# Performance work log

Measured on AMD Instinct MI355X. Metric: run time of the kernel, lower is better.

Reference implementation:

```python
import jax, jax.numpy as jnp
import numpy as np

NUM_HEADS = 16
HEAD_DIM = 64
MAX_MEM = 4 * 4096
TOP_K = 8
EPS = 1e-8


def _l2norm(x, eps=EPS):
    # matches torch F.normalize(p=2, dim=-1, eps): x / max(||x||, eps)
    n = jnp.sqrt(jnp.sum(x * x, axis=-1, keepdims=True))
    return x / jnp.maximum(n, eps)


def setup_inputs() -> dict:
    key0 = jax.random.key(0)
    ks = jax.random.split(key0, 8)
    B, S, D = 2, 512, 1024
    H, hd = NUM_HEADS, HEAD_DIM
    return {
        "inputs": jax.random.normal(ks[0], (B, S, D), dtype=jnp.float32),
        "query": jax.random.normal(ks[1], (B, H, S, hd), dtype=jnp.float32),
        "key": jax.random.normal(ks[2], (B, H, S, hd), dtype=jnp.float32),
        "value": jax.random.normal(ks[3], (B, H, S, hd), dtype=jnp.float32),
        "outputs": jax.random.normal(ks[4], (B, H, S, hd), dtype=jnp.float32),
        "gate": jnp.zeros((H,), dtype=jnp.float32),  # nn.Parameter init zeros
        "key_memories": jax.random.normal(ks[5], (H, MAX_MEM, hd), dtype=jnp.float32),
        "value_memories": jax.random.normal(ks[6], (H, MAX_MEM, hd), dtype=jnp.float32),
    }


def reference(inputs, query, key, value, outputs, gate, key_memories, value_memories):
    B, S, _ = inputs.shape
    H = query.shape[1]
    hd = HEAD_DIM

    # [B,H,S,d] -> [H, B*S, d]
    q = jnp.transpose(query, (1, 0, 2, 3)).reshape(H, B * S, hd)

    # --- KNN lookup (no_grad in original) ---
    qn = _l2norm(q)                    # [H, N, d]
    kn = _l2norm(key_memories)         # [H, M, d]
    sims = jnp.einsum("hnd,hmd->hnm", qn, kn) / jnp.sqrt(jnp.float32(hd))
    scores, indices = jax.lax.top_k(sims, TOP_K)  # [H, N, k]

    # gather memory values per head: [H, N, k, d]
    mem_vals = jax.vmap(lambda vm, ix: vm[ix])(value_memories, indices)

    # weighted sum over k neighbors
    weighted = jnp.sum(mem_vals * scores[..., None], axis=2)  # [H, N, d]
    weighted = weighted.reshape(H, B, S, hd).transpose(1, 0, 2, 3)  # [B,H,S,d]

    g = jax.nn.sigmoid(gate).reshape(1, H, 1, 1)
    out_dim = outputs.shape[-1]
    combined = g * weighted[..., :out_dim] + (1.0 - g) * outputs
    return combined
```

## Files before the change

### kernel.cpp

```cpp
#include <hip/hip_runtime.h>
#include <math.h>

#define NHEADS 16
#define HD 64
#define MMEM 16384
#define NQ 1024
#define SEQ 512
#define EPS 1e-8f
#define NPART 16
#define NT 32
#define NGRP 32
#define CMAX 8

typedef short bf16x8 __attribute__((ext_vector_type(8)));
typedef float f32x16 __attribute__((ext_vector_type(16)));

__device__ inline unsigned short f2bf(float f) {
    unsigned int u = __builtin_bit_cast(unsigned int, f);
    unsigned int r = (u + 0x7FFFu + ((u >> 16) & 1u)) >> 16;
    return (unsigned short)r;
}

#define SS(Q) (Q.x*Q.x + Q.y*Q.y + Q.z*Q.z + Q.w*Q.w)

__global__ __launch_bounds__(256)
void kprep_kernel(const float* __restrict__ kmem,
                  float* __restrict__ knr,
                  unsigned short* __restrict__ kbf) {
    __shared__ float ssl[256];
    const int tid = threadIdx.x;
    const int gid = blockIdx.x * 256 + tid;
    const int lane = gid & 63;
    const int ks   = (gid >> 6) & 3;
    const int t    = (gid >> 8) & 511;
    const int h    = gid >> 17;
    const int r    = lane & 31;
    const int hi   = lane >> 5;
    const int row  = t * 32 + r;
    const int d0   = ks * 16 + hi * 8;

    const float* src = kmem + (((size_t)h * MMEM + row) << 6) + d0;
    float4 v0 = *(const float4*)(src);
    float4 v1 = *(const float4*)(src + 4);
    ssl[tid] = SS(v0) + SS(v1);
    __syncthreads();
    float tot = ssl[r +   0] + ssl[r +  32] + ssl[r +  64] + ssl[r +  96]
              + ssl[r + 128] + ssl[r + 160] + ssl[r + 192] + ssl[r + 224];
    const float rn = 1.0f / fmaxf(sqrtf(tot), EPS);
    if (tid < 32) knr[h * MMEM + row] = rn;

    uint4 o;
    o.x = (unsigned)f2bf(v0.x * rn) | ((unsigned)f2bf(v0.y * rn) << 16);
    o.y = (unsigned)f2bf(v0.z * rn) | ((unsigned)f2bf(v0.w * rn) << 16);
    o.z = (unsigned)f2bf(v1.x * rn) | ((unsigned)f2bf(v1.y * rn) << 16);
    o.w = (unsigned)f2bf(v1.z * rn) | ((unsigned)f2bf(v1.w * rn) << 16);
    *(uint4*)(kbf + (size_t)gid * 8) = o;
}

__device__ inline float max16v(const f32x16& a) {
    float m0 = fmaxf(fmaxf(a[0],  a[1]),  a[2]);
    float m1 = fmaxf(fmaxf(a[3],  a[4]),  a[5]);
    float m2 = fmaxf(fmaxf(a[6],  a[7]),  a[8]);
    float m3 = fmaxf(fmaxf(a[9],  a[10]), a[11]);
    float m4 = fmaxf(fmaxf(a[12], a[13]), a[14]);
    float n0 = fmaxf(fmaxf(m0, m1), m2);
    float n1 = fmaxf(fmaxf(m3, m4), a[15]);
    return fmaxf(n0, n1);
}

__device__ inline void ins8(float (&tv)[8], float v) {
#pragma unroll
    for (int j = 0; j < 8; ++j) {
        float h_ = fmaxf(tv[j], v);
        float l_ = fminf(tv[j], v);
        tv[j] = h_;
        v = l_;
    }
}

__device__ inline void ins8u64(unsigned long long (&tv)[8], unsigned long long v) {
#pragma unroll
    for (int j = 0; j < 8; ++j) {
        unsigned long long h_ = tv[j] > v ? tv[j] : v;
        unsigned long long l_ = tv[j] > v ? v : tv[j];
        tv[j] = h_;
        v = l_;
    }
}

__device__ inline bf16x8 pack8f(float4 a, float4 b) {
    bf16x8 f;
    f[0] = (short)f2bf(a.x); f[1] = (short)f2bf(a.y);
    f[2] = (short)f2bf(a.z); f[3] = (short)f2bf(a.w);
    f[4] = (short)f2bf(b.x); f[5] = (short)f2bf(b.y);
    f[6] = (short)f2bf(b.z); f[7] = (short)f2bf(b.w);
    return f;
}

#define MFMA8Z(ACCA, ACCB, A0, A1, A2, A3)                                    \
    f32x16 ACCA = __builtin_amdgcn_mfma_f32_32x32x16_bf16(A0, qA[0], z16, 0,0,0); \
    f32x16 ACCB = __builtin_amdgcn_mfma_f32_32x32x16_bf16(A0, qB[0], z16, 0,0,0); \
    ACCA = __builtin_amdgcn_mfma_f32_32x32x16_bf16(A1, qA[1], ACCA, 0, 0, 0); \
    ACCB = __builtin_amdgcn_mfma_f32_32x32x16_bf16(A1, qB[1], ACCB, 0, 0, 0); \
    ACCA = __builtin_amdgcn_mfma_f32_32x32x16_bf16(A2, qA[2], ACCA, 0, 0, 0); \
    ACCB = __builtin_amdgcn_mfma_f32_32x32x16_bf16(A2, qB[2], ACCB, 0, 0, 0); \
    ACCA = __builtin_amdgcn_mfma_f32_32x32x16_bf16(A3, qA[3], ACCA, 0, 0, 0); \
    ACCB = __builtin_amdgcn_mfma_f32_32x32x16_bf16(A3, qB[3], ACCB, 0, 0, 0);

__global__ __launch_bounds__(64, 4)
void scanA_kernel(const float* __restrict__ query,
                  const unsigned short* __restrict__ kbf,
                  float* __restrict__ pmax) {
    const int lane = threadIdx.x;
    int bid = blockIdx.x;
    const int p  = bid & 15;  bid >>= 4;
    const int qg = bid & 15;  bid >>= 4;
    const int h  = bid;
    const int col = lane & 31;
    const int hi  = lane >> 5;
    const int n0  = qg * 64 + col;
    const int n1  = n0 + 32;

    bf16x8 qA[4], qB[4];
    {
        const int b0 = n0 >> 9, s0 = n0 & 511;
        const int b1 = n1 >> 9, s1 = n1 & 511;
        const float* qp0 = query + ((((size_t)b0 * NHEADS + h) * SEQ + s0) << 6);
        const float* qp1 = query + ((((size_t)b1 * NHEADS + h) * SEQ + s1) << 6);
#pragma unroll
        for (int ks = 0; ks < 4; ++ks) {
            const int d0 = ks * 16 + hi * 8;
            qA[ks] = pack8f(*(const float4*)(qp0 + d0), *(const float4*)(qp0 + d0 + 4));
            qB[ks] = pack8f(*(const float4*)(qp1 + d0), *(const float4*)(qp1 + d0 + 4));
        }
    }

    const f32x16 z16 = {0,0,0,0,0,0,0,0,0,0,0,0,0,0,0,0};
    float gA = -1e30f, gB = -1e30f;

    const unsigned char* ptr = (const unsigned char*)kbf
        + ((size_t)h * 512 + (size_t)p * NT) * 4096 + (size_t)lane * 16;

    bf16x8 aX0, aX1, aX2, aX3, aY0, aY1, aY2, aY3;
    aX0 = *(const bf16x8*)(ptr);
    aX1 = *(const bf16x8*)(ptr + 1024);
    aX2 = *(const bf16x8*)(ptr + 2048);
    aX3 = *(const bf16x8*)(ptr + 3072);

#pragma unroll 1
    for (int t = 0; t < NT; t += 2) {
        {
            const unsigned char* pn = ptr + (size_t)(t + 1) * 4096;
            aY0 = *(const bf16x8*)(pn);
            aY1 = *(const bf16x8*)(pn + 1024);
            aY2 = *(const bf16x8*)(pn + 2048);
            aY3 = *(const bf16x8*)(pn + 3072);
        }
        {
            MFMA8Z(accA, accB, aX0, aX1, aX2, aX3)
            gA = fmaxf(gA, max16v(accA));
            gB = fmaxf(gB, max16v(accB));
        }
        if (t + 2 < NT) {
            const unsigned char* p2 = ptr + (size_t)(t + 2) * 4096;
            aX0 = *(const bf16x8*)(p2);
            aX1 = *(const bf16x8*)(p2 + 1024);
            aX2 = *(const bf16x8*)(p2 + 2048);
            aX3 = *(const bf16x8*)(p2 + 3072);
        }
        {
            MFMA8Z(accC, accD, aY0, aY1, aY2, aY3)
            gA = fmaxf(gA, max16v(accC));
            gB = fmaxf(gB, max16v(accD));
        }
    }

    pmax[(((size_t)h * NQ + n0) << 5) + p * 2 + hi] = gA;
    pmax[(((size_t)h * NQ + n1) << 5) + p * 2 + hi] = gB;
}

__global__ __launch_bounds__(256)
void taured_kernel(const float* __restrict__ pmax,
                   float* __restrict__ tauv) {
    const int gid = blockIdx.x * 256 + threadIdx.x;
    float tv[8];
#pragma unroll
    for (int j = 0; j < 8; ++j) tv[j] = -1e30f;
#pragma unroll
    for (int k = 0; k < NGRP; ++k) ins8(tv, pmax[((size_t)gid << 5) + k]);
    tauv[gid] = tv[7];
}

__global__ __launch_bounds__(64, 4)
void scanB_kernel(const float* __restrict__ query,
                  const unsigned short* __restrict__ kbf,
                  const float* __restrict__ tauv,
                  unsigned* __restrict__ pcand,
                  unsigned* __restrict__ pcnt) {
    const int lane = threadIdx.x;
    int bid = blockIdx.x;
    const int p  = bid & 15;  bid >>= 4;
    const int qg = bid & 15;  bid >>= 4;
    const int h  = bid;
    const int col = lane & 31;
    const int hi  = lane >> 5;
    const int n0  = qg * 64 + col;
    const int n1  = n0 + 32;

    bf16x8 qA[4], qB[4];
    float ssA = 0.f, ssB = 0.f;
    {
        const int b0 = n0 >> 9, s0 = n0 & 511;
        const int b1 = n1 >> 9, s1 = n1 & 511;
        const float* qp0 = query + ((((size_t)b0 * NHEADS + h) * SEQ + s0) << 6);
        const float* qp1 = query + ((((size_t)b1 * NHEADS + h) * SEQ + s1) << 6);
#pragma unroll
        for (int ks = 0; ks < 4; ++ks) {
            const int d0 = ks * 16 + hi * 8;
            float4 a0 = *(const float4*)(qp0 + d0), b0v = *(const float4*)(qp0 + d0 + 4);
            float4 a1 = *(const float4*)(qp1 + d0), b1v = *(const float4*)(qp1 + d0 + 4);
            ssA += SS(a0) + SS(b0v);
            ssB += SS(a1) + SS(b1v);
            qA[ks] = pack8f(a0, b0v);
            qB[ks] = pack8f(a1, b1v);
        }
    }
    ssA += __shfl_xor(ssA, 32);
    ssB += __shfl_xor(ssB, 32);
    const float tA = tauv[h * NQ + n0] - (sqrtf(ssA) * 0.0078125f + 0.01f);
    const float tB = tauv[h * NQ + n1] - (sqrtf(ssB) * 0.0078125f + 0.01f);

    const f32x16 z16 = {0,0,0,0,0,0,0,0,0,0,0,0,0,0,0,0};

    const unsigned char* ptr = (const unsigned char*)kbf
        + ((size_t)h * 512 + (size_t)p * NT) * 4096 + (size_t)lane * 16;

    unsigned cA = 0, cB = 0;
    const size_t chA = (((size_t)h * NQ + n0) << 5) + p * 2 + hi;
    const size_t chB = (((size_t)h * NQ + n1) << 5) + p * 2 + hi;
    unsigned* mApt = pcand + chA * CMAX;
    unsigned* mBpt = pcand + chB * CMAX;

#define EMITG(ACC, TAU, C, LST, MBV) do {                                     \
        const float _g = max16v(ACC);                                         \
        if (_g >= (TAU)) {                                                    \
            unsigned _msk = 0;                                                \
            _Pragma("unroll")                                                 \
            for (int _r = 0; _r < 16; ++_r)                                   \
                _msk |= (ACC[_r] >= (TAU)) ? (1u << _r) : 0u;                 \
            do {                                                              \
                int _r = __ffs(_msk) - 1;                                     \
                unsigned _idx = (unsigned)((MBV) + (_r & 3) + 8 * (_r >> 2)); \
                if ((C) < CMAX) (LST)[C] = _idx;                              \
                ++(C);                                                        \
                _msk &= _msk - 1;                                             \
            } while (_msk);                                                   \
        }                                                                     \
    } while (0)

    bf16x8 aX0, aX1, aX2, aX3, aY0, aY1, aY2, aY3;
    aX0 = *(const bf16x8*)(ptr);
    aX1 = *(const bf16x8*)(ptr + 1024);
    aX2 = *(const bf16x8*)(ptr + 2048);
    aX3 = *(const bf16x8*)(ptr + 3072);

#pragma unroll 1
    for (int t = 0; t < NT; t += 2) {
        {
            const unsigned char* pn = ptr + (size_t)(t + 1) * 4096;
            aY0 = *(const bf16x8*)(pn);
            aY1 = *(const bf16x8*)(pn + 1024);
            aY2 = *(const bf16x8*)(pn + 2048);
            aY3 = *(const bf16x8*)(pn + 3072);
        }
        {
            MFMA8Z(accA, accB, aX0, aX1, aX2, aX3)
            const int mbv = p * 1024 + t * 32 + 4 * hi;
            EMITG(accA, tA, cA, mApt, mbv);
            EMITG(accB, tB, cB, mBpt, mbv);
        }
        if (t + 2 < NT) {
            const unsigned char* p2 = ptr + (size_t)(t + 2) * 4096;
            aX0 = *(const bf16x8*)(p2);
            aX1 = *(const bf16x8*)(p2 + 1024);
            aX2 = *(const bf16x8*)(p2 + 2048);
            aX3 = *(const bf16x8*)(p2 + 3072);
        }
        {
            MFMA8Z(accC, accD, aY0, aY1, aY2, aY3)
            const int mbv = p * 1024 + (t + 1) * 32 + 4 * hi;
            EMITG(accC, tA, cA, mApt, mbv);
            EMITG(accD, tB, cB, mBpt, mbv);
        }
    }
    pcnt[chA] = cA;
    pcnt[chB] = cB;
#undef EMITG
}

__global__ __launch_bounds__(64, 8)
void rescore_merge_kernel(const float* __restrict__ query,
                          const float* __restrict__ kmem,
                          const float* __restrict__ knr,
                          const unsigned* __restrict__ pcand,
                          const unsigned* __restrict__ pcnt,
                          const float* __restrict__ vmem,
                          const float* __restrict__ outputs,
                          const float* __restrict__ gate,
                          float* __restrict__ out) {
    __shared__ unsigned cands[NGRP * CMAX];
    const int gid = blockIdx.x;
    const int h = gid >> 10;
    const int n = gid & 1023;
    const int b = n >> 9;
    const int s = n & 511;
    const int lane = threadIdx.x;
    const int d4 = lane & 15;
    const int d5 = lane & 31;

    const float* qbase = query + ((((size_t)b * NHEADS + h) * SEQ + s) << 6);
    const float4 q4 = ((const float4*)qbase)[d4];
    float ssp = SS(q4);
    ssp += __shfl_xor(ssp, 1);
    ssp += __shfl_xor(ssp, 2);
    ssp += __shfl_xor(ssp, 4);
    ssp += __shfl_xor(ssp, 8);
    const float qs = 1.0f / (fmaxf(sqrtf(ssp), EPS) * 8.0f);

    const unsigned cg = pcnt[((size_t)gid << 5) + d5];
    const bool anyovf = (__ballot(cg > CMAX) != 0ULL);
    unsigned inc = cg;
#pragma unroll
    for (int d = 1; d < 32; d <<= 1) {
        unsigned t = __shfl_up(inc, d, 32);
        if (d5 >= d) inc += t;
    }
    const unsigned ct = __shfl(inc, 31, 32);
    const unsigned excl = inc - cg;
    if (lane < 32) {
        const unsigned* lp = pcand + (((size_t)gid << 5) + lane) * CMAX;
        const unsigned cc = cg > CMAX ? CMAX : cg;
        for (unsigned c = 0; c < cc; ++c) cands[excl + c] = lp[c];
    }
    __syncthreads();

    const float* kb = kmem + ((size_t)h << 20);
    const float* nb = knr + h * MMEM;

    unsigned long long top[8];
#pragma unroll
    for (int j = 0; j < 8; ++j) top[j] = 0ULL;

#define SCORE_KEY(IDX) ({                                                     \
        float4 kv = ((const float4*)(kb + ((size_t)(IDX) << 6)))[d4];         \
        float d = q4.x*kv.x + q4.y*kv.y + q4.z*kv.z + q4.w*kv.w;              \
        d += __shfl_xor(d, 1);                                                \
        d += __shfl_xor(d, 2);                                                \
        d += __shfl_xor(d, 4);                                                \
        d += __shfl_xor(d, 8);                                                \
        const float sc = d * qs * nb[IDX];                                    \
        unsigned su = __builtin_bit_cast(unsigned, sc);                       \
        unsigned ms = su ^ ((su >> 31) ? 0xFFFFFFFFu : 0x80000000u);          \
        ((unsigned long long)ms << 32) | (0xFFFFFFFFu - (unsigned)(IDX));     \
    })

    if (!anyovf) {
#pragma unroll 1
        for (unsigned c = 0; c < ct; ++c) {
            const unsigned idx = cands[c];
            ins8u64(top, SCORE_KEY(idx));
        }
    } else {
#pragma unroll 1
        for (int m = 0; m < MMEM; ++m) ins8u64(top, SCORE_KEY(m));
    }
#undef SCORE_KEY

    float acc = 0.0f;
    const float* vb = vmem + ((size_t)h << 20);
#pragma unroll
    for (int j = 0; j < 8; ++j) {
        const unsigned long long key = top[j];
        const unsigned idx = 0xFFFFFFFFu - (unsigned)(key & 0xFFFFFFFFu);
        const unsigned ms = (unsigned)(key >> 32);
        const unsigned su = ms ^ ((ms >> 31) ? 0x80000000u : 0xFFFFFFFFu);
        const float sc = __builtin_bit_cast(float, su);
        acc = fmaf(sc, vb[((size_t)idx << 6) + lane], acc);
    }

    const float gg = 1.0f / (1.0f + expf(-gate[h]));
    const size_t off = ((((size_t)b * NHEADS + h) * SEQ + s) << 6) + lane;
    out[off] = gg * acc + (1.0f - gg) * outputs[off];
}

__global__ void knorm_kernel(const float* __restrict__ kmem,
                             float* __restrict__ knr) {
    int gid = blockIdx.x * 256 + threadIdx.x;
    int mem = gid >> 4;
    int d4  = gid & 15;
    float4 kv = reinterpret_cast<const float4*>(kmem)[(size_t)mem * 16 + d4];
    float ss = SS(kv);
    ss += __shfl_xor(ss, 1);
    ss += __shfl_xor(ss, 2);
    ss += __shfl_xor(ss, 4);
    ss += __shfl_xor(ss, 8);
    if (d4 == 0) knr[mem] = 1.0f / fmaxf(sqrtf(ss), EPS);
}

__global__ __launch_bounds__(64, 4)
void scan_kernel(const float* __restrict__ query,
                 const float* __restrict__ kmem,
                 const float* __restrict__ knr,
                 float* __restrict__ pscore,
                 int* __restrict__ pidx,
                 int P, int CH) {
    const int lane = threadIdx.x & 63;
    int bid = blockIdx.x;
    const int p  = bid % P;  bid /= P;
    const int qb = bid & 15; bid >>= 4;
    const int h  = bid;
    const int n  = qb * 64 + lane;
    const int b  = n >> 9;
    const int s  = n & 511;

    const float4* qp = reinterpret_cast<const float4*>(
        query + (((size_t)b * NHEADS + h) * SEQ + s) * HD);
    float q[HD];
    float ss = 0.0f;
#pragma unroll
    for (int i = 0; i < 16; ++i) {
        float4 v = qp[i];
        q[4*i+0] = v.x; q[4*i+1] = v.y; q[4*i+2] = v.z; q[4*i+3] = v.w;
        ss += SS(v);
    }
    const float rq = 1.0f / (fmaxf(sqrtf(ss), EPS) * 8.0f);
#pragma unroll
    for (int i = 0; i < HD; ++i) q[i] *= rq;

    float tv[8]; int ti[8];
#pragma unroll
    for (int j = 0; j < 8; ++j) { tv[j] = -INFINITY; ti[j] = 0; }

    const int m0 = p * CH;
    const float4* kp = reinterpret_cast<const float4*>(
        kmem + ((size_t)h * MMEM + m0) * HD);
    const float* knrp = knr + h * MMEM + m0;

    for (int mm = 0; mm < CH; ++mm) {
        float d0 = 0.f, d1 = 0.f, d2 = 0.f, d3 = 0.f;
#pragma unroll
        for (int i = 0; i < 16; ++i) {
            float4 kv = kp[(size_t)mm * 16 + i];
            d0 = fmaf(q[4*i+0], kv.x, d0);
            d1 = fmaf(q[4*i+1], kv.y, d1);
            d2 = fmaf(q[4*i+2], kv.z, d2);
            d3 = fmaf(q[4*i+3], kv.w, d3);
        }
        const float sim = ((d0 + d1) + (d2 + d3)) * knrp[mm];
        if (sim > tv[7]) {
            tv[7] = sim; ti[7] = m0 + mm;
#pragma unroll
            for (int j = 7; j > 0; --j) {
                if (tv[j] > tv[j-1]) {
                    float tf = tv[j]; tv[j] = tv[j-1]; tv[j-1] = tf;
                    int   tu = ti[j]; ti[j] = ti[j-1]; ti[j-1] = tu;
                }
            }
        }
    }

    const size_t base = (((size_t)h * NQ + n) * P + p) * 8;
#pragma unroll
    for (int j = 0; j < 8; ++j) { pscore[base+j] = tv[j]; pidx[base+j] = ti[j]; }
}

__global__ void merge_kernel(const float* __restrict__ pscore,
                             const int* __restrict__ pidx,
                             const float* __restrict__ vmem,
                             const float* __restrict__ outputs,
                             const float* __restrict__ gate,
                             float* __restrict__ out, int P) {
    const int t = blockIdx.x * 256 + threadIdx.x;
    const int h = t >> 10;
    const int n = t & 1023;
    const int b = n >> 9;
    const int s = n & 511;

    float tv[8]; int ti[8];
    const size_t base = ((size_t)h * NQ + n) * P * 8;
#pragma unroll
    for (int j = 0; j < 8; ++j) { tv[j] = pscore[base + j]; ti[j] = pidx[base + j]; }
    const int total = P * 8;
    for (int c = 8; c < total; ++c) {
        const float v = pscore[base + c];
        if (v > tv[7]) {
            tv[7] = v; ti[7] = pidx[base + c];
#pragma unroll
            for (int j = 7; j > 0; --j) {
                if (tv[j] > tv[j-1]) {
                    float tf = tv[j]; tv[j] = tv[j-1]; tv[j-1] = tf;
                    int   tu = ti[j]; ti[j] = ti[j-1]; ti[j-1] = tu;
                }
            }
        }
    }

    float4 acc[16];
#pragma unroll
    for (int i = 0; i < 16; ++i) acc[i] = make_float4(0.f, 0.f, 0.f, 0.f);
#pragma unroll
    for (int j = 0; j < 8; ++j) {
        const float4* vp = reinterpret_cast<const float4*>(
            vmem + ((size_t)h * MMEM + ti[j]) * HD);
        const float sc = tv[j];
#pragma unroll
        for (int i = 0; i < 16; ++i) {
            float4 v = vp[i];
            acc[i].x = fmaf(sc, v.x, acc[i].x);
            acc[i].y = fmaf(sc, v.y, acc[i].y);
            acc[i].z = fmaf(sc, v.z, acc[i].z);
            acc[i].w = fmaf(sc, v.w, acc[i].w);
        }
    }

    const float g  = 1.0f / (1.0f + expf(-gate[h]));
    const float og = 1.0f - g;
    const size_t off = (((size_t)b * NHEADS + h) * SEQ + s) * HD;
    const float4* op = reinterpret_cast<const float4*>(outputs + off);
    float4* dst = reinterpret_cast<float4*>(out + off);
#pragma unroll
    for (int i = 0; i < 16; ++i) {
        float4 o = op[i];
        float4 r;
        r.x = g * acc[i].x + og * o.x;
        r.y = g * acc[i].y + og * o.y;
        r.z = g * acc[i].z + og * o.z;
        r.w = g * acc[i].w + og * o.w;
        dst[i] = r;
    }
}

extern "C" void kernel_launch(void* const* d_in, const int* in_sizes, int n_in,
                              void* d_out, int out_size, void* d_ws, size_t ws_size,
                              hipStream_t stream) {
    const float* query   = (const float*)d_in[1];
    const float* outputs = (const float*)d_in[4];
    const float* gate    = (const float*)d_in[5];
    const float* kmem    = (const float*)d_in[6];
    const float* vmem    = (const float*)d_in[7];
    float* out = (float*)d_out;

    const size_t NQTOT    = (size_t)NHEADS * NQ;
    const size_t sz_knr   = (size_t)NHEADS * MMEM * 4;
    const size_t sz_kbf   = (size_t)NHEADS * MMEM * HD * 2;
    const size_t sz_pmax  = NQTOT * NGRP * 4;
    const size_t sz_tauv  = NQTOT * 4;
    const size_t sz_pcand = NQTOT * NGRP * CMAX * 4;
    const size_t sz_pcnt  = NQTOT * NGRP * 4;
    const size_t need = sz_knr + sz_kbf + sz_pmax + sz_tauv + sz_pcand + sz_pcnt;

    if (ws_size >= need) {
        char* w = (char*)d_ws;
        float*          knr   = (float*)w;          w += sz_knr;
        unsigned short* kbf   = (unsigned short*)w; w += sz_kbf;
        float*          pmax  = (float*)w;          w += sz_pmax;
        float*          tauv  = (float*)w;          w += sz_tauv;
        unsigned*       pcand = (unsigned*)w;       w += sz_pcand;
        unsigned*       pcnt  = (unsigned*)w;

        kprep_kernel<<<(NHEADS * 512 * 4 * 64) / 256, 256, 0, stream>>>(kmem, knr, kbf);
        scanA_kernel<<<NHEADS * 16 * NPART, 64, 0, stream>>>(query, kbf, pmax);
        taured_kernel<<<(int)(NQTOT / 256), 256, 0, stream>>>(pmax, tauv);
        scanB_kernel<<<NHEADS * 16 * NPART, 64, 0, stream>>>(query, kbf, tauv, pcand, pcnt);
        rescore_merge_kernel<<<(int)NQTOT, 64, 0, stream>>>(
            query, kmem, knr, pcand, pcnt, vmem, outputs, gate, out);
    } else {
        int P = 16;
        while (P > 4 &&
               (size_t)NHEADS * MMEM * 4 + (size_t)NHEADS * NQ * (size_t)P * 64 > ws_size)
            P >>= 1;
        const int CH = MMEM / P;

        float* knr    = (float*)d_ws;
        float* pscore = knr + (size_t)NHEADS * MMEM;
        int*   pidx   = (int*)(pscore + (size_t)NHEADS * NQ * (size_t)P * 8);

        knorm_kernel<<<(NHEADS * MMEM * 16) / 256, 256, 0, stream>>>(kmem, knr);
        scan_kernel<<<NHEADS * 16 * P, 64, 0, stream>>>(
            query, kmem, knr, pscore, pidx, P, CH);
        merge_kernel<<<(NHEADS * NQ) / 256, 256, 0, stream>>>(
            pscore, pidx, vmem, outputs, gate, out, P);
    }
}
```

Before: 149.7 us.

## Share key tiles across four waves via double-buffered LDS staging in scan kernels

Both scan kernels now launch 256-thread blocks where four waves cover 256 queries of one head and partition. They share key-memory bf16 tiles staged into LDS through async global_load_lds with double buffering, instead of each 64-thread wave reading the same keys from global memory. This cuts redundant global/L2 key traffic by roughly four times, at the cost of a block-wide barrier per chunk, 32KB of LDS per block and fewer blocks in the grid.

```diff
diff --git a/kernel.cpp b/kernel.cpp
--- a/kernel.cpp
+++ b/kernel.cpp
@@ -11,9 +11,14 @@
 #define NT 32
 #define NGRP 32
 #define CMAX 8
+#define CHT 4
+#define NCHUNK 8
 
 typedef short bf16x8 __attribute__((ext_vector_type(8)));
 typedef float f32x16 __attribute__((ext_vector_type(16)));
+
+typedef const __attribute__((address_space(1))) unsigned int* gas_u32p;
+typedef __attribute__((address_space(3))) unsigned int* las_u32p;
 
 __device__ inline unsigned short f2bf(float f) {
     unsigned int u = __builtin_bit_cast(unsigned int, f);
@@ -107,18 +112,31 @@
     ACCA = __builtin_amdgcn_mfma_f32_32x32x16_bf16(A3, qA[3], ACCA, 0, 0, 0); \
     ACCB = __builtin_amdgcn_mfma_f32_32x32x16_bf16(A3, qB[3], ACCB, 0, 0, 0);
 
-__global__ __launch_bounds__(64, 4)
+#define STAGE(CH) do {                                                        \
+        const unsigned char* _s = gsrc + (size_t)(CH) * (CHT * 4096);         \
+        unsigned char* _d = &lds[(CH) & 1][0];                                \
+        _Pragma("unroll")                                                     \
+        for (int _j = 0; _j < CHT; ++_j)                                      \
+            __builtin_amdgcn_global_load_lds(                                 \
+                (gas_u32p)(const void*)(_s + _j * 4096 + tid * 16),           \
+                (las_u32p)(void*)(_d + _j * 4096 + tid * 16), 16, 0, 0);      \
+    } while (0)
+
+__global__ __launch_bounds__(256, 4)
 void scanA_kernel(const float* __restrict__ query,
                   const unsigned short* __restrict__ kbf,
                   float* __restrict__ pmax) {
-    const int lane = threadIdx.x;
+    __shared__ __align__(16) unsigned char lds[2][CHT * 4096];
+    const int tid  = threadIdx.x;
+    const int lane = tid & 63;
+    const int wid  = tid >> 6;
     int bid = blockIdx.x;
-    const int p  = bid & 15;  bid >>= 4;
-    const int qg = bid & 15;  bid >>= 4;
+    const int p  = bid & 15; bid >>= 4;
+    const int qb = bid & 3;  bid >>= 2;
     const int h  = bid;
     const int col = lane & 31;
     const int hi  = lane >> 5;
-    const int n0  = qg * 64 + col;
+    const int n0  = qb * 256 + wid * 64 + col;
     const int n1  = n0 + 32;
 
     bf16x8 qA[4], qB[4];
@@ -138,41 +156,27 @@
     const f32x16 z16 = {0,0,0,0,0,0,0,0,0,0,0,0,0,0,0,0};
     float gA = -1e30f, gB = -1e30f;
 
-    const unsigned char* ptr = (const unsigned char*)kbf
-        + ((size_t)h * 512 + (size_t)p * NT) * 4096 + (size_t)lane * 16;
-
-    bf16x8 aX0, aX1, aX2, aX3, aY0, aY1, aY2, aY3;
-    aX0 = *(const bf16x8*)(ptr);
-    aX1 = *(const bf16x8*)(ptr + 1024);
-    aX2 = *(const bf16x8*)(ptr + 2048);
-    aX3 = *(const bf16x8*)(ptr + 3072);
-
+    const unsigned char* gsrc = (const unsigned char*)kbf
+        + ((size_t)h * 512 + (size_t)p * NT) * 4096;
+
+    STAGE(0);
+    __syncthreads();
 #pragma unroll 1
-    for (int t = 0; t < NT; t += 2) {
-        {
-            const unsigned char* pn = ptr + (size_t)(t + 1) * 4096;
-            aY0 = *(const bf16x8*)(pn);
-            aY1 = *(const bf16x8*)(pn + 1024);
-            aY2 = *(const bf16x8*)(pn + 2048);
-            aY3 = *(const bf16x8*)(pn + 3072);
-        }
-        {
-            MFMA8Z(accA, accB, aX0, aX1, aX2, aX3)
+    for (int c = 0; c < NCHUNK; ++c) {
+        if (c + 1 < NCHUNK) STAGE(c + 1);
+        const unsigned char* base = &lds[c & 1][0];
+#pragma unroll
+        for (int t = 0; t < CHT; ++t) {
+            const unsigned char* tb = base + t * 4096 + lane * 16;
+            bf16x8 a0 = *(const bf16x8*)(tb);
+            bf16x8 a1 = *(const bf16x8*)(tb + 1024);
+            bf16x8 a2 = *(const bf16x8*)(tb + 2048);
+            bf16x8 a3 = *(const bf16x8*)(tb + 3072);
+            MFMA8Z(accA, accB, a0, a1, a2, a3)
             gA = fmaxf(gA, max16v(accA));
             gB = fmaxf(gB, max16v(accB));
         }
-        if (t + 2 < NT) {
-            const unsigned char* p2 = ptr + (size_t)(t + 2) * 4096;
-            aX0 = *(const bf16x8*)(p2);
-            aX1 = *(const bf16x8*)(p2 + 1024);
-            aX2 = *(const bf16x8*)(p2 + 2048);
-            aX3 = *(const bf16x8*)(p2 + 3072);
-        }
-        {
-            MFMA8Z(accC, accD, aY0, aY1, aY2, aY3)
-            gA = fmaxf(gA, max16v(accC));
-            gB = fmaxf(gB, max16v(accD));
-        }
+        __syncthreads();
     }
 
     pmax[(((size_t)h * NQ + n0) << 5) + p * 2 + hi] = gA;
@@ -191,20 +195,23 @@
     tauv[gid] = tv[7];
 }
 
-__global__ __launch_bounds__(64, 4)
+__global__ __launch_bounds__(256, 4)
 void scanB_kernel(const float* __restrict__ query,
                   const unsigned short* __restrict__ kbf,
                   const float* __restrict__ tauv,
                   unsigned* __restrict__ pcand,
                   unsigned* __restrict__ pcnt) {
-    const int lane = threadIdx.x;
+    __shared__ __align__(16) unsigned char lds[2][CHT * 4096];
+    const int tid  = threadIdx.x;
+    const int lane = tid & 63;
+    const int wid  = tid >> 6;
     int bid = blockIdx.x;
-    const int p  = bid & 15;  bid >>= 4;
-    const int qg = bid & 15;  bid >>= 4;
+    const int p  = bid & 15; bid >>= 4;
+    const int qb = bid & 3;  bid >>= 2;
     const int h  = bid;
     const int col = lane & 31;
     const int hi  = lane >> 5;
-    const int n0  = qg * 64 + col;
+    const int n0  = qb * 256 + wid * 64 + col;
     const int n1  = n0 + 32;
 
     bf16x8 qA[4], qB[4];
@@ -232,8 +239,8 @@
 
     const f32x16 z16 = {0,0,0,0,0,0,0,0,0,0,0,0,0,0,0,0};
 
-    const unsigned char* ptr = (const unsigned char*)kbf
-        + ((size_t)h * 512 + (size_t)p * NT) * 4096 + (size_t)lane * 16;
+    const unsigned char* gsrc = (const unsigned char*)kbf
+        + ((size_t)h * 512 + (size_t)p * NT) * 4096;
 
     unsigned cA = 0, cB = 0;
     const size_t chA = (((size_t)h * NQ + n0) << 5) + p * 2 + hi;
@@ -258,40 +265,25 @@
         }                                                                     \
     } while (0)
 
-    bf16x8 aX0, aX1, aX2, aX3, aY0, aY1, aY2, aY3;
-    aX0 = *(const bf16x8*)(ptr);
-    aX1 = *(const bf16x8*)(ptr + 1024);
-    aX2 = *(const bf16x8*)(ptr + 2048);
-    aX3 = *(const bf16x8*)(ptr + 3072);
-
+    STAGE(0);
+    __syncthreads();
 #pragma unroll 1
-    for (int t = 0; t < NT; t += 2) {
-        {
-            const unsigned char* pn = ptr + (size_t)(t + 1) * 4096;
-            aY0 = *(const bf16x8*)(pn);
-            aY1 = *(const bf16x8*)(pn + 1024);
-            aY2 = *(const bf16x8*)(pn + 2048);
-            aY3 = *(const bf16x8*)(pn + 3072);
-        }
-        {
-            MFMA8Z(accA, accB, aX0, aX1, aX2, aX3)
-            const int mbv = p * 1024 + t * 32 + 4 * hi;
+    for (int c = 0; c < NCHUNK; ++c) {
+        if (c + 1 < NCHUNK) STAGE(c + 1);
+        const unsigned char* base = &lds[c & 1][0];
+#pragma unroll
+        for (int t = 0; t < CHT; ++t) {
+            const unsigned char* tb = base + t * 4096 + lane * 16;
+            bf16x8 a0 = *(const bf16x8*)(tb);
+            bf16x8 a1 = *(const bf16x8*)(tb + 1024);
+            bf16x8 a2 = *(const bf16x8*)(tb + 2048);
+            bf16x8 a3 = *(const bf16x8*)(tb + 3072);
+            MFMA8Z(accA, accB, a0, a1, a2, a3)
+            const int mbv = p * 1024 + (c * CHT + t) * 32 + 4 * hi;
             EMITG(accA, tA, cA, mApt, mbv);
             EMITG(accB, tB, cB, mBpt, mbv);
         }
-        if (t + 2 < NT) {
-            const unsigned char* p2 = ptr + (size_t)(t + 2) * 4096;
-            aX0 = *(const bf16x8*)(p2);
-            aX1 = *(const bf16x8*)(p2 + 1024);
-            aX2 = *(const bf16x8*)(p2 + 2048);
-            aX3 = *(const bf16x8*)(p2 + 3072);
-        }
-        {
-            MFMA8Z(accC, accD, aY0, aY1, aY2, aY3)
-            const int mbv = p * 1024 + (t + 1) * 32 + 4 * hi;
-            EMITG(accC, tA, cA, mApt, mbv);
-            EMITG(accD, tB, cB, mBpt, mbv);
-        }
+        __syncthreads();
     }
     pcnt[chA] = cA;
     pcnt[chB] = cB;
@@ -569,9 +561,9 @@
         unsigned*       pcnt  = (unsigned*)w;
 
         kprep_kernel<<<(NHEADS * 512 * 4 * 64) / 256, 256, 0, stream>>>(kmem, knr, kbf);
-        scanA_kernel<<<NHEADS * 16 * NPART, 64, 0, stream>>>(query, kbf, pmax);
+        scanA_kernel<<<NHEADS * 4 * NPART, 256, 0, stream>>>(query, kbf, pmax);
         taured_kernel<<<(int)(NQTOT / 256), 256, 0, stream>>>(pmax, tauv);
-        scanB_kernel<<<NHEADS * 16 * NPART, 64, 0, stream>>>(query, kbf, tauv, pcand, pcnt);
+        scanB_kernel<<<NHEADS * 4 * NPART, 256, 0, stream>>>(query, kbf, tauv, pcand, pcnt);
         rescore_merge_kernel<<<(int)NQTOT, 64, 0, stream>>>(
             query, kmem, knr, pcand, pcnt, vmem, outputs, gate, out);
     } else {
```

Result: faster. 145.6 us (-2.7%).
